# Optimization experiments

Measured on AMD Instinct MI355X. Metric: run time of the kernel, lower is better.

The kernel has to match this reference:

```python
import jax, jax.numpy as jnp
import numpy as np

N_NODES = 50000
N_EDGES = 800000
IN_DIM = 128
HID_DIM = 128
OUT_DIM = 128
NUM_GRAPHS = 64
NUM_CLASSES = 3


def _glorot(key, shape):
    lim = np.sqrt(6.0 / (shape[0] + shape[1])).astype(np.float32)
    return jax.random.uniform(key, shape, jnp.float32, -lim, lim)


def setup_inputs() -> dict:
    key = jax.random.key(0)
    ks = jax.random.split(key, 10)
    x = jax.random.normal(ks[0], (N_NODES, IN_DIM), jnp.float32)
    edge_index = jax.random.randint(ks[1], (2, N_EDGES), 0, N_NODES, jnp.int32).astype(jnp.int64)
    batch = jnp.sort(jax.random.randint(ks[2], (N_NODES,), 0, NUM_GRAPHS, jnp.int32)).astype(jnp.int64)
    return {
        "x": x,
        "edge_index": edge_index,
        "batch": batch,
        "W1": _glorot(ks[3], (IN_DIM, HID_DIM)),  "b1": jnp.zeros((HID_DIM,), jnp.float32),
        "W2": _glorot(ks[4], (HID_DIM, HID_DIM)), "b2": jnp.zeros((HID_DIM,), jnp.float32),
        "W3": _glorot(ks[5], (HID_DIM, OUT_DIM)), "b3": jnp.zeros((OUT_DIM,), jnp.float32),
        "C1": _glorot(ks[6], (OUT_DIM, HID_DIM)), "bc1": jnp.zeros((HID_DIM,), jnp.float32),
        "C2": _glorot(ks[7], (HID_DIM, NUM_CLASSES)), "bc2": jnp.zeros((NUM_CLASSES,), jnp.float32),
    }


def _gcn_conv(x, src, dst, norm, W, b):
    # PyG GCNConv: linear transform, then normalized gather/scatter aggregation, then bias.
    h = x @ W                               # [N, F_out]
    msg = h[src] * norm[:, None]            # [E+N, F_out] irregular gather
    return jax.ops.segment_sum(msg, dst, num_segments=N_NODES) + b


def reference(x, edge_index, batch, W1, b1, W2, b2, W3, b3, C1, bc1, C2, bc2):
    loops = jnp.arange(N_NODES, dtype=edge_index.dtype)
    src = jnp.concatenate([edge_index[0], loops])  # add self-loops as in GCNConv
    dst = jnp.concatenate([edge_index[1], loops])
    deg = jax.ops.segment_sum(jnp.ones_like(dst, jnp.float32), dst, num_segments=N_NODES)
    dinv = jnp.where(deg > 0, jax.lax.rsqrt(deg), 0.0)
    norm = dinv[src] * dinv[dst]            # symmetric D^-1/2 (A+I) D^-1/2 weights

    # dropout(p=0.2) is identity at inference time
    h = jax.nn.relu(_gcn_conv(x, src, dst, norm, W1, b1))
    h = jax.nn.relu(_gcn_conv(h, src, dst, norm, W2, b2))
    h = _gcn_conv(h, src, dst, norm, W3, b3)

    # global mean pool over batch segment ids
    counts = jax.ops.segment_sum(jnp.ones((N_NODES,), jnp.float32), batch, num_segments=NUM_GRAPHS)
    pooled = jax.ops.segment_sum(h, batch, num_segments=NUM_GRAPHS) / jnp.maximum(counts, 1.0)[:, None]

    g = jax.nn.relu(pooled @ C1 + bc1)      # classifier MLP (dropout 0.3 inactive)
    return g @ C2 + bc2                     # [NUM_GRAPHS, 3]
```

## Files before the change

### kernel.cpp

```cpp
#include <hip/hip_runtime.h>
#include <hip/hip_bf16.h>

#define N_NODES    50000
#define DIM        128
#define NUM_GRAPHS 64
#define NUM_CLASSES 3
#define NPAD       50176
#define XPITCH     136

typedef unsigned short ushort_t;
typedef unsigned int   uint_t;
typedef __attribute__((ext_vector_type(8))) short short8;
typedef __attribute__((ext_vector_type(4))) float f32x4;

__device__ __forceinline__ ushort_t f2bf(float f) {
    union { float f; uint_t u; } v; v.f = f;
    uint_t r = v.u + 0x7fffu + ((v.u >> 16) & 1u);
    return (ushort_t)(r >> 16);
}
__device__ __forceinline__ float bflo(uint_t u) {
    union { uint_t u; float f; } v; v.u = u << 16; return v.f;
}
__device__ __forceinline__ float bfhi(uint_t u) {
    union { uint_t u; float f; } v; v.u = u & 0xffff0000u; return v.f;
}

__device__ __forceinline__ void gather_raw(
    int n, int lane, const int* __restrict__ rowptr,
    const int* __restrict__ csr_src, const uint_t* __restrict__ Tb,
    float2& acc)
{
    int p0 = rowptr[n], p1 = rowptr[n + 1];
    uint_t us = Tb[n * 64 + lane];
    float2 a0 = make_float2(bflo(us), bfhi(us));
    float2 a1 = make_float2(0.f, 0.f);
    int p = p0;
    int nb = (p1 - p0) >> 3;
    if (nb > 0) {
        uint_t ucur[8];
        #pragma unroll
        for (int q = 0; q < 8; ++q) ucur[q] = Tb[csr_src[p + q] * 64 + lane];
        for (int b = 1; b < nb; ++b) {
            uint_t unxt[8];
            #pragma unroll
            for (int q = 0; q < 8; ++q) unxt[q] = Tb[csr_src[p + 8 + q] * 64 + lane];
            #pragma unroll
            for (int q = 0; q < 8; q += 2) {
                a0.x += bflo(ucur[q]);     a0.y += bfhi(ucur[q]);
                a1.x += bflo(ucur[q + 1]); a1.y += bfhi(ucur[q + 1]);
            }
            #pragma unroll
            for (int q = 0; q < 8; ++q) ucur[q] = unxt[q];
            p += 8;
        }
        #pragma unroll
        for (int q = 0; q < 8; q += 2) {
            a0.x += bflo(ucur[q]);     a0.y += bfhi(ucur[q]);
            a1.x += bflo(ucur[q + 1]); a1.y += bfhi(ucur[q + 1]);
        }
        p += 8;
    }
    for (; p + 4 <= p1; p += 4) {
        int s[4]; uint_t u[4];
        #pragma unroll
        for (int q = 0; q < 4; ++q) s[q] = csr_src[p + q];
        #pragma unroll
        for (int q = 0; q < 4; ++q) u[q] = Tb[s[q] * 64 + lane];
        #pragma unroll
        for (int q = 0; q < 4; q += 2) {
            a0.x += bflo(u[q]);     a0.y += bfhi(u[q]);
            a1.x += bflo(u[q + 1]); a1.y += bfhi(u[q + 1]);
        }
    }
    for (; p < p1; ++p) {
        int s = csr_src[p];
        uint_t u = Tb[s * 64 + lane];
        a0.x += bflo(u); a0.y += bfhi(u);
    }
    acc.x += a0.x + a1.x;
    acc.y += a0.y + a1.y;
}

__global__ void k_init(int* degi, float* pooled, float* counts) {
    int i = blockIdx.x * 256 + threadIdx.x;
    if (i < NPAD) degi[i] = 0;
    if (i < NUM_GRAPHS * DIM) pooled[i] = 0.0f;
    if (i < NUM_GRAPHS) counts[i] = 0.0f;
}

__global__ void k_prep(const float* __restrict__ W1, const float* __restrict__ W2,
                       const float* __restrict__ W3, ushort_t* __restrict__ Wt) {
    int i = blockIdx.x * 256 + threadIdx.x;
    int mat = i >> 14;
    int idx = i & 16383;
    const float* W = (mat == 0) ? W1 : (mat == 1) ? W2 : W3;
    int n = idx >> 7, k = idx & 127;
    Wt[mat * 16384 + n * 128 + k] = f2bf(W[k * 128 + n]);
}

__global__ void k_count(const int* __restrict__ dst, int* degi, int* rank, int nedges) {
    int e = blockIdx.x * 256 + threadIdx.x;
    if (e < nedges) rank[e] = atomicAdd(&degi[dst[e]], 1);
}

__global__ __launch_bounds__(256) void k_scan1(const int* __restrict__ degi,
                                               int* rowptr, int* bsum) {
    __shared__ int sh[256];
    int i = blockIdx.x * 256 + threadIdx.x;
    int v = degi[i];
    sh[threadIdx.x] = v;
    __syncthreads();
    for (int off = 1; off < 256; off <<= 1) {
        int t = (threadIdx.x >= off) ? sh[threadIdx.x - off] : 0;
        __syncthreads();
        sh[threadIdx.x] += t;
        __syncthreads();
    }
    rowptr[i] = sh[threadIdx.x] - v;
    if (threadIdx.x == 255) bsum[blockIdx.x] = sh[255];
}

__global__ __launch_bounds__(256) void k_scan2(int* bsum, int nblocks) {
    __shared__ int sh[256];
    int v = (threadIdx.x < nblocks) ? bsum[threadIdx.x] : 0;
    sh[threadIdx.x] = v;
    __syncthreads();
    for (int off = 1; off < 256; off <<= 1) {
        int t = (threadIdx.x >= off) ? sh[threadIdx.x - off] : 0;
        __syncthreads();
        sh[threadIdx.x] += t;
        __syncthreads();
    }
    if (threadIdx.x < nblocks) bsum[threadIdx.x] = sh[threadIdx.x] - v;
}

__global__ __launch_bounds__(256) void k_scan3(int* rowptr, const int* __restrict__ bsum,
                                               const int* __restrict__ degi,
                                               float* dinv) {
    int i = blockIdx.x * 256 + threadIdx.x;
    rowptr[i] = rowptr[i] + bsum[blockIdx.x];
    if (i < N_NODES) dinv[i] = rsqrtf((float)degi[i] + 1.0f);
}

__global__ void k_fill(const int* __restrict__ src, const int* __restrict__ dst,
                       const int* __restrict__ rank, const int* __restrict__ rowptr,
                       int* csr_src, int nedges) {
    int e = blockIdx.x * 256 + threadIdx.x;
    if (e < nedges) csr_src[rowptr[dst[e]] + rank[e]] = src[e];
}

__global__ __launch_bounds__(256) void k_mm1(
    const float* __restrict__ xin, const ushort_t* __restrict__ WtG,
    const float* __restrict__ dinv, ushort_t* __restrict__ TbOut)
{
    __shared__ ushort_t Wl[DIM * XPITCH];
    __shared__ ushort_t Xl[64 * XPITCH];

    const int tid = threadIdx.x;
    const int rowbase = blockIdx.x * 64;

    #pragma unroll
    for (int i = 0; i < 8; ++i) {
        int g = tid + i * 256;
        uint4 v = ((const uint4*)WtG)[g];
        *((uint4*)&Wl[(g >> 4) * XPITCH + (g & 15) * 8]) = v;
    }
    #pragma unroll
    for (int i = 0; i < 8; ++i) {
        int c = tid + i * 256;
        int row = c >> 5;
        int grow = rowbase + row;
        float4 f = make_float4(0.f, 0.f, 0.f, 0.f);
        if (grow < N_NODES)
            f = ((const float4*)xin)[(long long)rowbase * 32 + c];
        ushort4 h;
        h.x = f2bf(f.x); h.y = f2bf(f.y); h.z = f2bf(f.z); h.w = f2bf(f.w);
        *((ushort4*)&Xl[row * XPITCH + (c & 31) * 4]) = h;
    }
    __syncthreads();

    const int wave = tid >> 6;
    const int lane = tid & 63;
    const int quad = lane >> 4;
    const int lm   = lane & 15;
    const int m0   = wave * 16;

    short8 af[4];
    #pragma unroll
    for (int k0 = 0; k0 < 4; ++k0)
        af[k0] = *(const short8*)&Xl[(m0 + lm) * XPITCH + k0 * 32 + quad * 8];

    int noder[4]; float di[4]; bool okr[4];
    #pragma unroll
    for (int r = 0; r < 4; ++r) {
        noder[r] = rowbase + m0 + quad * 4 + r;
        okr[r] = (noder[r] < N_NODES);
        di[r] = okr[r] ? dinv[noder[r]] : 0.f;
    }

    for (int n0 = 0; n0 < DIM; n0 += 16) {
        f32x4 acc = {0.f, 0.f, 0.f, 0.f};
        #pragma unroll
        for (int k0 = 0; k0 < 4; ++k0) {
            short8 bf = *(const short8*)&Wl[(n0 + lm) * XPITCH + k0 * 32 + quad * 8];
            acc = __builtin_amdgcn_mfma_f32_16x16x32_bf16(af[k0], bf, acc, 0, 0, 0);
        }
        int n = n0 + lm;
        #pragma unroll
        for (int r = 0; r < 4; ++r)
            if (okr[r])
                TbOut[(long long)noder[r] * DIM + n] = f2bf(acc[r] * di[r]);
    }
}

__global__ __launch_bounds__(1024) void k_fused(
    const int* __restrict__ rowptr, const int* __restrict__ csr_src,
    const float* __restrict__ dinv, const uint_t* __restrict__ TbIn,
    const ushort_t* __restrict__ WtG, const float* __restrict__ b_prev,
    ushort_t* __restrict__ TbOut)
{
    __shared__ ushort_t Xl[16 * XPITCH];

    const int tid = threadIdx.x;
    const int rowbase = blockIdx.x * 16;
    const int wave = tid >> 6;
    const int lane = tid & 63;

    float2 bias2 = ((const float2*)b_prev)[lane];

    {
        int r = wave;
        int n = rowbase + r;
        float2 acc = make_float2(0.f, 0.f);
        float dd = 0.f;
        if (n < N_NODES) {
            dd = dinv[n];
            gather_raw(n, lane, rowptr, csr_src, TbIn, acc);
        }
        ushort2 h;
        h.x = f2bf(fmaxf(bias2.x + acc.x * dd, 0.f));
        h.y = f2bf(fmaxf(bias2.y + acc.y * dd, 0.f));
        *((ushort2*)&Xl[r * XPITCH + lane * 2]) = h;
    }
    __syncthreads();

    if (wave < 8) {
        const int quad = lane >> 4;
        const int lm   = lane & 15;

        short8 af[4];
        #pragma unroll
        for (int k0 = 0; k0 < 4; ++k0)
            af[k0] = *(const short8*)&Xl[lm * XPITCH + k0 * 32 + quad * 8];

        int noder[4]; float di[4]; bool okr[4];
        #pragma unroll
        for (int r = 0; r < 4; ++r) {
            noder[r] = rowbase + quad * 4 + r;
            okr[r] = (noder[r] < N_NODES);
            di[r] = okr[r] ? dinv[noder[r]] : 0.f;
        }

        const int n0 = wave * 16;
        f32x4 acc = {0.f, 0.f, 0.f, 0.f};
        #pragma unroll
        for (int k0 = 0; k0 < 4; ++k0) {
            short8 bf = *(const short8*)&WtG[(n0 + lm) * DIM + k0 * 32 + quad * 8];
            acc = __builtin_amdgcn_mfma_f32_16x16x32_bf16(af[k0], bf, acc, 0, 0, 0);
        }
        int n = n0 + lm;
        #pragma unroll
        for (int r = 0; r < 4; ++r)
            if (okr[r])
                TbOut[(long long)noder[r] * DIM + n] = f2bf(acc[r] * di[r]);
    }
}

__global__ __launch_bounds__(256) void k_poolgather(
    const int* __restrict__ rowptr, const int* __restrict__ csr_src,
    const float* __restrict__ dinv, const uint_t* __restrict__ Tb,
    const float* __restrict__ b3, const int* __restrict__ batch,
    float* pooled, float* counts)
{
    __shared__ float lp[8][DIM];
    __shared__ float lc[8];

    const int tid  = threadIdx.x;
    const int wave = tid >> 6;
    const int lane = tid & 63;
    const int blk0 = blockIdx.x * 16;

    #pragma unroll
    for (int i = 0; i < 4; ++i) ((float*)lp)[tid + i * 256] = 0.f;
    if (tid < 8) lc[tid] = 0.f;
    __syncthreads();

    const int gbase = batch[min(blk0, N_NODES - 1)];
    int n0 = blk0 + wave * 4;

    if (n0 < N_NODES) {
        int nend = min(n0 + 4, N_NODES);
        float2 bias2 = ((const float2*)b3)[lane];
        int cur = batch[n0];
        int runstart = n0;
        float2 pacc = make_float2(0.f, 0.f);

        for (int n = n0; n < nend; ++n) {
            int g = batch[n];
            if (g != cur) {
                int slot = cur - gbase;
                if (slot < 8) {
                    atomicAdd(&lp[slot][2 * lane], pacc.x);
                    atomicAdd(&lp[slot][2 * lane + 1], pacc.y);
                    if (lane == 0) atomicAdd(&lc[slot], (float)(n - runstart));
                } else {
                    atomicAdd(&pooled[cur * DIM + 2 * lane], pacc.x);
                    atomicAdd(&pooled[cur * DIM + 2 * lane + 1], pacc.y);
                    if (lane == 0) atomicAdd(&counts[cur], (float)(n - runstart));
                }
                pacc.x = 0.f; pacc.y = 0.f; cur = g; runstart = n;
            }
            float2 acc = make_float2(0.f, 0.f);
            gather_raw(n, lane, rowptr, csr_src, Tb, acc);
            float dd = dinv[n];
            pacc.x += bias2.x + acc.x * dd;
            pacc.y += bias2.y + acc.y * dd;
        }
        int slot = cur - gbase;
        if (slot < 8) {
            atomicAdd(&lp[slot][2 * lane], pacc.x);
            atomicAdd(&lp[slot][2 * lane + 1], pacc.y);
            if (lane == 0) atomicAdd(&lc[slot], (float)(nend - runstart));
        } else {
            atomicAdd(&pooled[cur * DIM + 2 * lane], pacc.x);
            atomicAdd(&pooled[cur * DIM + 2 * lane + 1], pacc.y);
            if (lane == 0) atomicAdd(&counts[cur], (float)(nend - runstart));
        }
    }
    __syncthreads();

    #pragma unroll
    for (int s = 0; s < 8; ++s) {
        if (lc[s] != 0.f) {
            if (tid < DIM) atomicAdd(&pooled[(gbase + s) * DIM + tid], lp[s][tid]);
            if (tid == DIM) atomicAdd(&counts[gbase + s], lc[s]);
        }
    }
}

__global__ __launch_bounds__(128) void k_cls(
    const float* __restrict__ pooled, const float* __restrict__ counts,
    const float* __restrict__ C1, const float* __restrict__ bc1,
    const float* __restrict__ C2, const float* __restrict__ bc2,
    float* out)
{
    __shared__ float pm[DIM];
    __shared__ float gv[DIM];
    int g = blockIdx.x, j = threadIdx.x;
    float cnt = fmaxf(counts[g], 1.0f);
    pm[j] = pooled[g * DIM + j] / cnt;
    __syncthreads();
    float a = bc1[j];
    for (int k = 0; k < DIM; ++k) a += pm[k] * C1[k * DIM + j];
    gv[j] = fmaxf(a, 0.f);
    __syncthreads();
    if (j < NUM_CLASSES) {
        float o = bc2[j];
        for (int k = 0; k < DIM; ++k) o += gv[k] * C2[k * NUM_CLASSES + j];
        out[g * NUM_CLASSES + j] = o;
    }
}

extern "C" void kernel_launch(void* const* d_in, const int* in_sizes, int n_in,
                              void* d_out, int out_size, void* d_ws, size_t ws_size,
                              hipStream_t stream) {
    const float* x    = (const float*)d_in[0];
    const int*   ei   = (const int*)d_in[1];
    const int*   batch= (const int*)d_in[2];
    const float* W1   = (const float*)d_in[3];
    const float* b1   = (const float*)d_in[4];
    const float* W2   = (const float*)d_in[5];
    const float* b2   = (const float*)d_in[6];
    const float* W3   = (const float*)d_in[7];
    const float* b3   = (const float*)d_in[8];
    const float* C1   = (const float*)d_in[9];
    const float* bc1  = (const float*)d_in[10];
    const float* C2   = (const float*)d_in[11];
    const float* bc2  = (const float*)d_in[12];

    const int nedges = in_sizes[1] / 2;
    const int* src = ei;
    const int* dst = ei + nedges;

    float*    dinv    = (float*)d_ws;
    uint_t*   TbA     = (uint_t*)(dinv + NPAD);
    uint_t*   TbB     = TbA + (long long)N_NODES * 64;
    float*    pooled  = (float*)(TbB + (long long)N_NODES * 64);
    float*    counts  = pooled + NUM_GRAPHS * DIM;
    int*      degi    = (int*)(counts + 64);
    int*      rowptr  = degi + NPAD;
    int*      bsum    = rowptr + NPAD + 256;
    int*      rank    = bsum + 256;
    int*      csr_src = rank + nedges;
    ushort_t* Wt      = (ushort_t*)(csr_src + nedges);

    const int nodeBlocks = NPAD / 256;
    const int mmBlocks   = (N_NODES + 63) / 64;
    const int fusedBlocks= (N_NODES + 15) / 16;
    const int pgBlocks   = (N_NODES + 15) / 16;
    const int edgeBlocks = (nedges + 255) / 256;

    k_init<<<nodeBlocks, 256, 0, stream>>>(degi, pooled, counts);
    k_prep<<<192, 256, 0, stream>>>(W1, W2, W3, Wt);
    k_count<<<edgeBlocks, 256, 0, stream>>>(dst, degi, rank, nedges);
    k_scan1<<<nodeBlocks, 256, 0, stream>>>(degi, rowptr, bsum);
    k_scan2<<<1, 256, 0, stream>>>(bsum, nodeBlocks);
    k_scan3<<<nodeBlocks, 256, 0, stream>>>(rowptr, bsum, degi, dinv);
    k_fill<<<edgeBlocks, 256, 0, stream>>>(src, dst, rank, rowptr, csr_src, nedges);

    k_mm1<<<mmBlocks, 256, 0, stream>>>(x, Wt, dinv, (ushort_t*)TbA);
    k_fused<<<fusedBlocks, 1024, 0, stream>>>(rowptr, csr_src, dinv, TbA,
                                              Wt + 16384, b1, (ushort_t*)TbB);
    k_fused<<<fusedBlocks, 1024, 0, stream>>>(rowptr, csr_src, dinv, TbB,
                                              Wt + 32768, b2, (ushort_t*)TbA);
    k_poolgather<<<pgBlocks, 256, 0, stream>>>(rowptr, csr_src, dinv, TbA,
                                               b3, batch, pooled, counts);
    k_cls<<<NUM_GRAPHS, 128, 0, stream>>>(pooled, counts, C1, bc1, C2, bc2,
                                          (float*)d_out);
}
```

Before: 323.0 us.

## Split feature tables into 32-column panels for cache-friendly neighbor gathers

Stores the bf16 node feature tables as four 32-column panels (node-major within each panel), so each gather block touches only a 64-byte slice per neighbor and the panel working set is more likely to stay in cache. The gather now uses 4 edges × 16 lanes per wave with a shuffle reduction, and it is split out of the fused gather+GEMM kernel into separate k_pgather and k_mm kernels that go through an intermediate panel buffer. The cost is extra launches, an additional write and read of the aggregated features, and four passes over the CSR indices.

```diff
diff --git a/kernel.cpp b/kernel.cpp
--- a/kernel.cpp
+++ b/kernel.cpp
@@ -7,6 +7,7 @@
 #define NUM_CLASSES 3
 #define NPAD       50176
 #define XPITCH     136
+#define PSTRIDE    (NPAD * 16)
 
 typedef unsigned short ushort_t;
 typedef unsigned int   uint_t;
@@ -25,60 +26,40 @@
     union { uint_t u; float f; } v; v.u = u & 0xffff0000u; return v.f;
 }
 
-__device__ __forceinline__ void gather_raw(
-    int n, int lane, const int* __restrict__ rowptr,
-    const int* __restrict__ csr_src, const uint_t* __restrict__ Tb,
-    float2& acc)
-{
+__device__ __forceinline__ float2 panel_gather(
+    int n, int e, int c, const int* __restrict__ rowptr,
+    const int* __restrict__ csr_src, const uint_t* __restrict__ Tp)
+{
+    float ax = 0.f, ay = 0.f;
     int p0 = rowptr[n], p1 = rowptr[n + 1];
-    uint_t us = Tb[n * 64 + lane];
-    float2 a0 = make_float2(bflo(us), bfhi(us));
-    float2 a1 = make_float2(0.f, 0.f);
     int p = p0;
     int nb = (p1 - p0) >> 3;
     if (nb > 0) {
-        uint_t ucur[8];
-        #pragma unroll
-        for (int q = 0; q < 8; ++q) ucur[q] = Tb[csr_src[p + q] * 64 + lane];
+        int s0 = csr_src[p + e], s1 = csr_src[p + 4 + e];
+        uint_t u0 = Tp[s0 * 16 + c], u1 = Tp[s1 * 16 + c];
         for (int b = 1; b < nb; ++b) {
-            uint_t unxt[8];
-            #pragma unroll
-            for (int q = 0; q < 8; ++q) unxt[q] = Tb[csr_src[p + 8 + q] * 64 + lane];
-            #pragma unroll
-            for (int q = 0; q < 8; q += 2) {
-                a0.x += bflo(ucur[q]);     a0.y += bfhi(ucur[q]);
-                a1.x += bflo(ucur[q + 1]); a1.y += bfhi(ucur[q + 1]);
-            }
-            #pragma unroll
-            for (int q = 0; q < 8; ++q) ucur[q] = unxt[q];
-            p += 8;
-        }
-        #pragma unroll
-        for (int q = 0; q < 8; q += 2) {
-            a0.x += bflo(ucur[q]);     a0.y += bfhi(ucur[q]);
-            a1.x += bflo(ucur[q + 1]); a1.y += bfhi(ucur[q + 1]);
-        }
+            int t0 = csr_src[p + 8 + e], t1 = csr_src[p + 12 + e];
+            uint_t v0 = Tp[t0 * 16 + c], v1 = Tp[t1 * 16 + c];
+            ax += bflo(u0) + bflo(u1);
+            ay += bfhi(u0) + bfhi(u1);
+            u0 = v0; u1 = v1; p += 8;
+        }
+        ax += bflo(u0) + bflo(u1);
+        ay += bfhi(u0) + bfhi(u1);
         p += 8;
     }
-    for (; p + 4 <= p1; p += 4) {
-        int s[4]; uint_t u[4];
-        #pragma unroll
-        for (int q = 0; q < 4; ++q) s[q] = csr_src[p + q];
-        #pragma unroll
-        for (int q = 0; q < 4; ++q) u[q] = Tb[s[q] * 64 + lane];
-        #pragma unroll
-        for (int q = 0; q < 4; q += 2) {
-            a0.x += bflo(u[q]);     a0.y += bfhi(u[q]);
-            a1.x += bflo(u[q + 1]); a1.y += bfhi(u[q + 1]);
-        }
-    }
-    for (; p < p1; ++p) {
-        int s = csr_src[p];
-        uint_t u = Tb[s * 64 + lane];
-        a0.x += bflo(u); a0.y += bfhi(u);
-    }
-    acc.x += a0.x + a1.x;
-    acc.y += a0.y + a1.y;
+    int cnt = p1 - p;
+    if (cnt > 0) {
+        uint_t u0 = 0, u1 = 0;
+        if (e < cnt)     { int s = csr_src[p + e];     u0 = Tp[s * 16 + c]; }
+        if (4 + e < cnt) { int s = csr_src[p + 4 + e]; u1 = Tp[s * 16 + c]; }
+        ax += bflo(u0) + bflo(u1);
+        ay += bfhi(u0) + bfhi(u1);
+    }
+    ax += __shfl_xor(ax, 16); ax += __shfl_xor(ax, 32);
+    ay += __shfl_xor(ay, 16); ay += __shfl_xor(ay, 32);
+    uint_t us = Tp[n * 16 + c];
+    return make_float2(ax + bflo(us), ay + bfhi(us));
 }
 
 __global__ void k_init(int* degi, float* pooled, float* counts) {
@@ -206,144 +187,196 @@
             acc = __builtin_amdgcn_mfma_f32_16x16x32_bf16(af[k0], bf, acc, 0, 0, 0);
         }
         int n = n0 + lm;
+        int pn = n >> 5;
         #pragma unroll
         for (int r = 0; r < 4; ++r)
             if (okr[r])
-                TbOut[(long long)noder[r] * DIM + n] = f2bf(acc[r] * di[r]);
-    }
-}
-
-__global__ __launch_bounds__(1024) void k_fused(
+                TbOut[(size_t)(pn * NPAD + noder[r]) * 32 + (n & 31)] =
+                    f2bf(acc[r] * di[r]);
+    }
+}
+
+__global__ __launch_bounds__(256) void k_pgather(
     const int* __restrict__ rowptr, const int* __restrict__ csr_src,
-    const float* __restrict__ dinv, const uint_t* __restrict__ TbIn,
-    const ushort_t* __restrict__ WtG, const float* __restrict__ b_prev,
-    ushort_t* __restrict__ TbOut)
-{
-    __shared__ ushort_t Xl[16 * XPITCH];
-
-    const int tid = threadIdx.x;
-    const int rowbase = blockIdx.x * 16;
+    const float* __restrict__ dinv, const uint_t* __restrict__ Tbp,
+    const float* __restrict__ b_prev, uint_t* __restrict__ Xg)
+{
+    const int tid  = threadIdx.x;
     const int wave = tid >> 6;
     const int lane = tid & 63;
-
-    float2 bias2 = ((const float2*)b_prev)[lane];
-
-    {
-        int r = wave;
-        int n = rowbase + r;
-        float2 acc = make_float2(0.f, 0.f);
-        float dd = 0.f;
+    const int e    = lane >> 4;
+    const int c    = lane & 15;
+    const int pan  = blockIdx.x & 3;
+    const int base = (blockIdx.x >> 2) * 32 + wave * 8;
+
+    const uint_t* Tp = Tbp + (size_t)pan * PSTRIDE;
+    uint_t*       Xp = Xg  + (size_t)pan * PSTRIDE;
+    float2 bb = ((const float2*)b_prev)[pan * 16 + c];
+
+    #pragma unroll 1
+    for (int i = 0; i < 8; ++i) {
+        int n = base + i;
+        float ax = 0.f, ay = 0.f;
         if (n < N_NODES) {
-            dd = dinv[n];
-            gather_raw(n, lane, rowptr, csr_src, TbIn, acc);
-        }
-        ushort2 h;
-        h.x = f2bf(fmaxf(bias2.x + acc.x * dd, 0.f));
-        h.y = f2bf(fmaxf(bias2.y + acc.y * dd, 0.f));
-        *((ushort2*)&Xl[r * XPITCH + lane * 2]) = h;
-    }
-    __syncthreads();
-
-    if (wave < 8) {
-        const int quad = lane >> 4;
-        const int lm   = lane & 15;
-
-        short8 af[4];
-        #pragma unroll
-        for (int k0 = 0; k0 < 4; ++k0)
-            af[k0] = *(const short8*)&Xl[lm * XPITCH + k0 * 32 + quad * 8];
-
-        int noder[4]; float di[4]; bool okr[4];
-        #pragma unroll
-        for (int r = 0; r < 4; ++r) {
-            noder[r] = rowbase + quad * 4 + r;
-            okr[r] = (noder[r] < N_NODES);
-            di[r] = okr[r] ? dinv[noder[r]] : 0.f;
-        }
-
-        const int n0 = wave * 16;
+            float2 a = panel_gather(n, e, c, rowptr, csr_src, Tp);
+            float dd = dinv[n];
+            ax = fmaxf(bb.x + a.x * dd, 0.f);
+            ay = fmaxf(bb.y + a.y * dd, 0.f);
+        }
+        if (e == 0) {
+            uint_t hx = f2bf(ax), hy = f2bf(ay);
+            __builtin_nontemporal_store((hy << 16) | hx, &Xp[n * 16 + c]);
+        }
+    }
+}
+
+__global__ __launch_bounds__(256) void k_mm(
+    const uint_t* __restrict__ Xg, const ushort_t* __restrict__ WtG,
+    const float* __restrict__ dinv, ushort_t* __restrict__ TbOut)
+{
+    __shared__ ushort_t Wl[DIM * XPITCH];
+    __shared__ ushort_t Xl[64 * XPITCH];
+
+    const int tid = threadIdx.x;
+    const int rowbase = blockIdx.x * 64;
+
+    #pragma unroll
+    for (int i = 0; i < 8; ++i) {
+        int g = tid + i * 256;
+        uint4 v = ((const uint4*)WtG)[g];
+        *((uint4*)&Wl[(g >> 4) * XPITCH + (g & 15) * 8]) = v;
+    }
+    #pragma unroll
+    for (int i = 0; i < 4; ++i) {
+        int g = tid + i * 256;
+        int r = g >> 4, rem = g & 15, pq = rem >> 2, q = rem & 3;
+        uint4 v = ((const uint4*)Xg)[(size_t)(pq * NPAD + rowbase + r) * 4 + q];
+        *((uint4*)&Xl[r * XPITCH + pq * 32 + q * 8]) = v;
+    }
+    __syncthreads();
+
+    const int wave = tid >> 6;
+    const int lane = tid & 63;
+    const int quad = lane >> 4;
+    const int lm   = lane & 15;
+    const int m0   = wave * 16;
+
+    short8 af[4];
+    #pragma unroll
+    for (int k0 = 0; k0 < 4; ++k0)
+        af[k0] = *(const short8*)&Xl[(m0 + lm) * XPITCH + k0 * 32 + quad * 8];
+
+    int noder[4]; float di[4]; bool okr[4];
+    #pragma unroll
+    for (int r = 0; r < 4; ++r) {
+        noder[r] = rowbase + m0 + quad * 4 + r;
+        okr[r] = (noder[r] < N_NODES);
+        di[r] = okr[r] ? dinv[noder[r]] : 0.f;
+    }
+
+    for (int n0 = 0; n0 < DIM; n0 += 16) {
         f32x4 acc = {0.f, 0.f, 0.f, 0.f};
         #pragma unroll
         for (int k0 = 0; k0 < 4; ++k0) {
-            short8 bf = *(const short8*)&WtG[(n0 + lm) * DIM + k0 * 32 + quad * 8];
+            short8 bf = *(const short8*)&Wl[(n0 + lm) * XPITCH + k0 * 32 + quad * 8];
             acc = __builtin_amdgcn_mfma_f32_16x16x32_bf16(af[k0], bf, acc, 0, 0, 0);
         }
         int n = n0 + lm;
+        int pn = n >> 5;
         #pragma unroll
         for (int r = 0; r < 4; ++r)
             if (okr[r])
-                TbOut[(long long)noder[r] * DIM + n] = f2bf(acc[r] * di[r]);
-    }
-}
-
-__global__ __launch_bounds__(256) void k_poolgather(
+                TbOut[(size_t)(pn * NPAD + noder[r]) * 32 + (n & 31)] =
+                    f2bf(acc[r] * di[r]);
+    }
+}
+
+__global__ __launch_bounds__(256) void k_ppool(
     const int* __restrict__ rowptr, const int* __restrict__ csr_src,
-    const float* __restrict__ dinv, const uint_t* __restrict__ Tb,
+    const float* __restrict__ dinv, const uint_t* __restrict__ Tbp,
     const float* __restrict__ b3, const int* __restrict__ batch,
     float* pooled, float* counts)
 {
     __shared__ float lp[8][DIM];
     __shared__ float lc[8];
+    __shared__ int   used[8];
 
     const int tid  = threadIdx.x;
     const int wave = tid >> 6;
     const int lane = tid & 63;
-    const int blk0 = blockIdx.x * 16;
+    const int e    = lane >> 4;
+    const int c    = lane & 15;
+    const int pan  = blockIdx.x & 3;
+    const int blk0 = (blockIdx.x >> 2) * 32;
+
+    const uint_t* Tp = Tbp + (size_t)pan * PSTRIDE;
+    const int ch = pan * 32 + 2 * c;
 
     #pragma unroll
     for (int i = 0; i < 4; ++i) ((float*)lp)[tid + i * 256] = 0.f;
-    if (tid < 8) lc[tid] = 0.f;
+    if (tid < 8) { lc[tid] = 0.f; used[tid] = 0; }
     __syncthreads();
 
     const int gbase = batch[min(blk0, N_NODES - 1)];
-    int n0 = blk0 + wave * 4;
+    int n0 = blk0 + wave * 8;
 
     if (n0 < N_NODES) {
-        int nend = min(n0 + 4, N_NODES);
-        float2 bias2 = ((const float2*)b3)[lane];
+        int nend = min(n0 + 8, N_NODES);
+        float2 bb = ((const float2*)b3)[pan * 16 + c];
         int cur = batch[n0];
         int runstart = n0;
-        float2 pacc = make_float2(0.f, 0.f);
+        float px = 0.f, py = 0.f;
 
         for (int n = n0; n < nend; ++n) {
             int g = batch[n];
             if (g != cur) {
                 int slot = cur - gbase;
                 if (slot < 8) {
-                    atomicAdd(&lp[slot][2 * lane], pacc.x);
-                    atomicAdd(&lp[slot][2 * lane + 1], pacc.y);
-                    if (lane == 0) atomicAdd(&lc[slot], (float)(n - runstart));
+                    if (e == 0) {
+                        atomicAdd(&lp[slot][ch], px);
+                        atomicAdd(&lp[slot][ch + 1], py);
+                        used[slot] = 1;
+                    }
+                    if (lane == 0 && pan == 0) atomicAdd(&lc[slot], (float)(n - runstart));
                 } else {
-                    atomicAdd(&pooled[cur * DIM + 2 * lane], pacc.x);
-                    atomicAdd(&pooled[cur * DIM + 2 * lane + 1], pacc.y);
-                    if (lane == 0) atomicAdd(&counts[cur], (float)(n - runstart));
+                    if (e == 0) {
+                        atomicAdd(&pooled[cur * DIM + ch], px);
+                        atomicAdd(&pooled[cur * DIM + ch + 1], py);
+                    }
+                    if (lane == 0 && pan == 0) atomicAdd(&counts[cur], (float)(n - runstart));
                 }
-                pacc.x = 0.f; pacc.y = 0.f; cur = g; runstart = n;
+                px = 0.f; py = 0.f; cur = g; runstart = n;
             }
-            float2 acc = make_float2(0.f, 0.f);
-            gather_raw(n, lane, rowptr, csr_src, Tb, acc);
+            float2 a = panel_gather(n, e, c, rowptr, csr_src, Tp);
             float dd = dinv[n];
-            pacc.x += bias2.x + acc.x * dd;
-            pacc.y += bias2.y + acc.y * dd;
+            px += bb.x + a.x * dd;
+            py += bb.y + a.y * dd;
         }
         int slot = cur - gbase;
         if (slot < 8) {
-            atomicAdd(&lp[slot][2 * lane], pacc.x);
-            atomicAdd(&lp[slot][2 * lane + 1], pacc.y);
-            if (lane == 0) atomicAdd(&lc[slot], (float)(nend - runstart));
+            if (e == 0) {
+                atomicAdd(&lp[slot][ch], px);
+                atomicAdd(&lp[slot][ch + 1], py);
+                used[slot] = 1;
+            }
+            if (lane == 0 && pan == 0) atomicAdd(&lc[slot], (float)(nend - runstart));
         } else {
-            atomicAdd(&pooled[cur * DIM + 2 * lane], pacc.x);
-            atomicAdd(&pooled[cur * DIM + 2 * lane + 1], pacc.y);
-            if (lane == 0) atomicAdd(&counts[cur], (float)(nend - runstart));
+            if (e == 0) {
+                atomicAdd(&pooled[cur * DIM + ch], px);
+                atomicAdd(&pooled[cur * DIM + ch + 1], py);
+            }
+            if (lane == 0 && pan == 0) atomicAdd(&counts[cur], (float)(nend - runstart));
         }
     }
     __syncthreads();
 
     #pragma unroll
     for (int s = 0; s < 8; ++s) {
-        if (lc[s] != 0.f) {
-            if (tid < DIM) atomicAdd(&pooled[(gbase + s) * DIM + tid], lp[s][tid]);
-            if (tid == DIM) atomicAdd(&counts[gbase + s], lc[s]);
+        if (used[s]) {
+            if (tid < 32) atomicAdd(&pooled[(gbase + s) * DIM + pan * 32 + tid],
+                                    lp[s][pan * 32 + tid]);
+            if (tid == 32 && pan == 0 && lc[s] != 0.f)
+                atomicAdd(&counts[gbase + s], lc[s]);
         }
     }
 }
@@ -394,8 +427,9 @@
 
     float*    dinv    = (float*)d_ws;
     uint_t*   TbA     = (uint_t*)(dinv + NPAD);
-    uint_t*   TbB     = TbA + (long long)N_NODES * 64;
-    float*    pooled  = (float*)(TbB + (long long)N_NODES * 64);
+    uint_t*   TbB     = TbA + (size_t)NPAD * 64;
+    uint_t*   Xb      = TbB + (size_t)NPAD * 64;
+    float*    pooled  = (float*)(Xb + (size_t)NPAD * 64);
     float*    counts  = pooled + NUM_GRAPHS * DIM;
     int*      degi    = (int*)(counts + 64);
     int*      rowptr  = degi + NPAD;
@@ -406,8 +440,7 @@
 
     const int nodeBlocks = NPAD / 256;
     const int mmBlocks   = (N_NODES + 63) / 64;
-    const int fusedBlocks= (N_NODES + 15) / 16;
-    const int pgBlocks   = (N_NODES + 15) / 16;
+    const int panBlocks  = (NPAD / 32) * 4;
     const int edgeBlocks = (nedges + 255) / 256;
 
     k_init<<<nodeBlocks, 256, 0, stream>>>(degi, pooled, counts);
@@ -419,12 +452,15 @@
     k_fill<<<edgeBlocks, 256, 0, stream>>>(src, dst, rank, rowptr, csr_src, nedges);
 
     k_mm1<<<mmBlocks, 256, 0, stream>>>(x, Wt, dinv, (ushort_t*)TbA);
-    k_fused<<<fusedBlocks, 1024, 0, stream>>>(rowptr, csr_src, dinv, TbA,
-                                              Wt + 16384, b1, (ushort_t*)TbB);
-    k_fused<<<fusedBlocks, 1024, 0, stream>>>(rowptr, csr_src, dinv, TbB,
-                                              Wt + 32768, b2, (ushort_t*)TbA);
-    k_poolgather<<<pgBlocks, 256, 0, stream>>>(rowptr, csr_src, dinv, TbA,
-                                               b3, batch, pooled, counts);
+
+    k_pgather<<<panBlocks, 256, 0, stream>>>(rowptr, csr_src, dinv, TbA, b1, Xb);
+    k_mm<<<mmBlocks, 256, 0, stream>>>(Xb, Wt + 16384, dinv, (ushort_t*)TbB);
+
+    k_pgather<<<panBlocks, 256, 0, stream>>>(rowptr, csr_src, dinv, TbB, b2, Xb);
+    k_mm<<<mmBlocks, 256, 0, stream>>>(Xb, Wt + 32768, dinv, (ushort_t*)TbA);
+
+    k_ppool<<<panBlocks, 256, 0, stream>>>(rowptr, csr_src, dinv, TbA,
+                                           b3, batch, pooled, counts);
     k_cls<<<NUM_GRAPHS, 128, 0, stream>>>(pooled, counts, C1, bc1, C2, bc2,
                                           (float*)d_out);
 }
```

Measured after the change: 403.4 us. 24.9% more time.
